# Performance work log

Hardware: AMD Instinct MI355X
Metric: run time of the kernel (lower is better)

The kernel has to match this reference:

```python
import jax, jax.numpy as jnp
import numpy as np

D_MODEL = 1024
HEADS = 16
HEAD_DIM = D_MODEL // HEADS


def setup_inputs() -> dict:
    key = jax.random.key(0)
    ks = jax.random.split(key, 6)
    B, S, D = 2, 2048, D_MODEL
    scale = 1.0 / np.sqrt(D)
    x = jax.random.normal(ks[0], (B, S, D), dtype=jnp.float32)
    mask = jax.random.randint(ks[1], (B, S), 0, 2, dtype=jnp.int32)
    Wq = jax.random.normal(ks[2], (D, D), dtype=jnp.float32) * scale
    Wk = jax.random.normal(ks[3], (D, D), dtype=jnp.float32) * scale
    Wv = jax.random.normal(ks[4], (D, D), dtype=jnp.float32) * scale
    Wp = jax.random.normal(ks[5], (D, D), dtype=jnp.float32) * scale
    zb = jnp.zeros((D,), dtype=jnp.float32)
    return {"x": x, "mask": mask, "Wq": Wq, "bq": zb, "Wk": Wk, "bk": zb,
            "Wv": Wv, "bv": zb, "Wp": Wp, "bp": zb}


def reference(x, mask, Wq, bq, Wk, bk, Wv, bv, Wp, bp):
    B, S, D = x.shape
    H, Dh = HEADS, HEAD_DIM

    def split_heads(t):  # [B,S,D] -> [B,H,S,Dh]
        return t.reshape(B, S, H, Dh).transpose(0, 2, 1, 3)

    q = split_heads(x @ Wq + bq)
    k = split_heads(x @ Wk + bk)
    v = split_heads(x @ Wv + bv)

    att = jnp.einsum('bhqd,bhkd->bhqk', q, k) / jnp.sqrt(jnp.float32(Dh))
    # key-padding mask: [B,S] -> [B,1,1,S]; masked positions -> -inf
    m = (mask[:, None, None, :] != 0)
    att = jnp.where(m, att, -jnp.inf)
    att = jax.nn.softmax(att, axis=-1)
    # rows that were fully masked produce NaN -> zero them (masked_fill(isnan, 0))
    att = jnp.where(jnp.isnan(att), 0.0, att)

    y = jnp.einsum('bhqk,bhkd->bhqd', att, v)  # [B,H,S,Dh]
    y = y.transpose(0, 2, 1, 3).reshape(B, S, D)
    return y @ Wp + bp
```

## Files before the change

kernel.cpp:

```cpp
#include <hip/hip_runtime.h>
#include <math.h>

#define D_MODEL 1024
#define HEADS 16
#define HEAD_DIM 64
#define SEQ 2048
#define BATCH 2
#define KVT 64
#define QTILE 64
#define SCALE_Q 0.18033688f

typedef __attribute__((ext_vector_type(8))) short bf16x8;
typedef __attribute__((ext_vector_type(4))) float f32x4;

__device__ __forceinline__ short f2bf(float f) {
    union { float f; unsigned u; } v; v.f = f;
    unsigned r = (v.u + 0x7FFFu + ((v.u >> 16) & 1u)) >> 16;
    return (short)r;
}

__device__ __forceinline__ unsigned cvt_pk_bf16(float lo, float hi) {
    unsigned r;
    asm("v_cvt_pk_bf16_f32 %0, %1, %2" : "=v"(r) : "v"(lo), "v"(hi));
    return r;
}

__device__ __forceinline__ float fexp2(float x) {
    float r;
    asm("v_exp_f32 %0, %1" : "=v"(r) : "v"(x));
    return r;
}

__global__ __launch_bounds__(256) void prep(
    const float* __restrict__ x, const float* __restrict__ Wq,
    const float* __restrict__ Wk, const float* __restrict__ Wv,
    const float* __restrict__ Wp, const int* __restrict__ mask,
    short* __restrict__ xb, short* __restrict__ Wqkvt,
    short* __restrict__ Wpt, float* __restrict__ maskf) {
    __shared__ float t[32][33];
    const int bid = blockIdx.x;
    if (bid < 2048) {
        const int i = bid * 256 + threadIdx.x;
        float4 a = ((const float4*)x)[2 * i];
        float4 b = ((const float4*)x)[2 * i + 1];
        short r[8] = {f2bf(a.x), f2bf(a.y), f2bf(a.z), f2bf(a.w),
                      f2bf(b.x), f2bf(b.y), f2bf(b.z), f2bf(b.w)};
        *(uint4*)(xb + 8 * i) = *(uint4*)r;
    } else if (bid < 6144) {
        const int tt = bid - 2048;
        const int z = tt >> 10;
        const int rem = tt & 1023;
        const float* W = z == 0 ? Wq : z == 1 ? Wk : z == 2 ? Wv : Wp;
        short* dst = (z < 3) ? Wqkvt + (size_t)z * 1024 * 1024 : Wpt;
        const int n0 = (rem & 31) * 32, k0 = (rem >> 5) * 32;
        const int tx = threadIdx.x & 31, ty = threadIdx.x >> 5;
#pragma unroll
        for (int j = 0; j < 4; ++j)
            t[ty + j * 8][tx] = W[(size_t)(k0 + ty + j * 8) * 1024 + n0 + tx];
        __syncthreads();
#pragma unroll
        for (int j = 0; j < 4; ++j) {
            const int n = ty + j * 8;
            dst[(size_t)(n0 + n) * 1024 + k0 + tx] = f2bf(t[tx][n]);
        }
    } else {
        const int i = (bid - 6144) * 256 + threadIdx.x;
        maskf[i] = mask[i] ? 0.f : -INFINITY;
    }
}

template <int MODE>
__global__ __launch_bounds__(256) void mfma_gemm(
    const short* __restrict__ A, const short* __restrict__ Bt,
    const float* __restrict__ b0, const float* __restrict__ b1,
    const float* __restrict__ b2, float* __restrict__ outf,
    short* __restrict__ o0, short* __restrict__ o1, short* __restrict__ o2,
    int M, int N, int K) {
    __shared__ short As[2 * 128 * 32];
    __shared__ short Bs[2 * 128 * 32];

    const int tid = threadIdx.x;
    const int wave = tid >> 6, lane = tid & 63;
    const int l15 = lane & 15, lhi = lane >> 4;
    const int wm = wave >> 1, wn = wave & 1;

    const int nwgx = gridDim.x;
    const int nwg = nwgx * gridDim.y;
    const int lin = blockIdx.y * nwgx + blockIdx.x;
    const int swz = (lin & 7) * (nwg >> 3) + (lin >> 3);
    const int bm0 = (swz / nwgx) * 128, bn0 = (swz % nwgx) * 128;

    f32x4 acc[4][4];
#pragma unroll
    for (int m = 0; m < 4; ++m)
#pragma unroll
        for (int n = 0; n < 4; ++n) acc[m][n] = (f32x4){0.f, 0.f, 0.f, 0.f};

#define STAGE_G(buf, kt_)                                                         \
    {                                                                             \
        const int k0 = (kt_) * 32;                                                \
        _Pragma("unroll") for (int p = 0; p < 2; ++p) {                           \
            const int o = (wave * 2 + p) * 64 + lane;                             \
            const int r = o >> 2;                                                 \
            const int gs = (o & 3) ^ ((r >> 1) & 3);                              \
            __builtin_amdgcn_global_load_lds(                                     \
                (const __attribute__((address_space(1))) void*)(                  \
                    A + (size_t)(bm0 + r) * K + k0 + gs * 8),                     \
                (__attribute__((address_space(3))) void*)(                        \
                    As + (size_t)(buf) * 4096 + (wave * 2 + p) * 512),            \
                16, 0, 0);                                                        \
            __builtin_amdgcn_global_load_lds(                                     \
                (const __attribute__((address_space(1))) void*)(                  \
                    Bt + (size_t)(bn0 + r) * K + k0 + gs * 8),                    \
                (__attribute__((address_space(3))) void*)(                        \
                    Bs + (size_t)(buf) * 4096 + (wave * 2 + p) * 512),            \
                16, 0, 0);                                                        \
        }                                                                         \
    }

    const int NT = K / 32;
    STAGE_G(0, 0);
    __syncthreads();
    for (int kt = 0; kt < NT; ++kt) {
        const int cur = kt & 1;
        if (kt + 1 < NT) STAGE_G((kt + 1) & 1, kt + 1);
        bf16x8 af[4], bf[4];
        const int sg = (lhi ^ ((l15 >> 1) & 3)) * 16;
#pragma unroll
        for (int m = 0; m < 4; ++m)
            af[m] = *(const bf16x8*)((char*)As + cur * 8192 +
                                     (wm * 64 + m * 16 + l15) * 64 + sg);
#pragma unroll
        for (int n = 0; n < 4; ++n)
            bf[n] = *(const bf16x8*)((char*)Bs + cur * 8192 +
                                     (wn * 64 + n * 16 + l15) * 64 + sg);
        __builtin_amdgcn_s_setprio(1);
#pragma unroll
        for (int m = 0; m < 4; ++m)
#pragma unroll
            for (int n = 0; n < 4; ++n)
                acc[m][n] = __builtin_amdgcn_mfma_f32_16x16x32_bf16(af[m], bf[n], acc[m][n], 0, 0, 0);
        __builtin_amdgcn_s_setprio(0);
        __syncthreads();
    }
#undef STAGE_G

    const int which = (MODE == 1) ? (bn0 >> 10) : 0;
#pragma unroll
    for (int m = 0; m < 4; ++m) {
#pragma unroll
        for (int n = 0; n < 4; ++n) {
            const int col = bn0 + wn * 64 + n * 16 + l15;
            if (MODE == 0) {
#pragma unroll
                for (int rr = 0; rr < 4; ++rr) {
                    const int row = bm0 + wm * 64 + m * 16 + lhi * 4 + rr;
                    outf[(size_t)row * N + col] = acc[m][n][rr] + b0[col];
                }
            } else {
                const int cc = col & 1023;
                const int h = cc >> 6, dh = cc & 63;
                const int row0 = bm0 + wm * 64 + m * 16 + lhi * 4;
                const int b = row0 >> 11, s0 = row0 & (SEQ - 1);
                if (which == 2) {
                    const float bias = b2[cc];
                    uint2 w;
                    w.x = cvt_pk_bf16(acc[m][n][0] + bias, acc[m][n][1] + bias);
                    w.y = cvt_pk_bf16(acc[m][n][2] + bias, acc[m][n][3] + bias);
                    *(uint2*)(o2 + ((size_t)(b * HEADS + h) * HEAD_DIM + dh) * SEQ + s0) = w;
                } else {
                    const float bias = (which == 0 ? b0 : b1)[cc];
                    short* dst = which == 0 ? o0 : o1;
#pragma unroll
                    for (int rr = 0; rr < 4; ++rr) {
                        float v = acc[m][n][rr] + bias;
                        if (which == 0) v *= SCALE_Q;
                        dst[(((size_t)(b * HEADS + h)) * SEQ + s0 + rr) * HEAD_DIM + dh] = f2bf(v);
                    }
                }
            }
        }
    }
}

__global__ __launch_bounds__(256, 4) void flash_attn(
    const short* __restrict__ Q, const short* __restrict__ K,
    const short* __restrict__ Vt, const float* __restrict__ maskf,
    short* __restrict__ Y) {
    __shared__ unsigned char kt[2][KVT * 128];
    __shared__ unsigned char vt[2][HEAD_DIM * 128];
    __shared__ unsigned char pb[4][16 * 128];

    const int tid = threadIdx.x;
    const int wave = tid >> 6;
    const int lane = tid & 63;
    const int l15 = lane & 15;
    const int lhi = lane >> 4;

    const int nwg = gridDim.x;
    const int wg = blockIdx.x;
    const int swz = (wg & 7) * (nwg >> 3) + (wg >> 3);
    const int qt = swz & 31;
    const int bh = swz >> 5;
    const int b = bh >> 4;

    const int q0 = qt * QTILE + wave * 16;

    const short* Qp = Q + ((size_t)bh * SEQ + q0 + l15) * HEAD_DIM;
    bf16x8 qf[2];
    qf[0] = *(const bf16x8*)(Qp + 8 * lhi);
    qf[1] = *(const bf16x8*)(Qp + 8 * lhi + 32);

    const unsigned char* Kb8 = (const unsigned char*)(K + (size_t)bh * SEQ * HEAD_DIM);
    const unsigned char* Vb8 = (const unsigned char*)(Vt + (size_t)bh * HEAD_DIM * SEQ);
    const float* mb = maskf + b * SEQ;

#define STAGE(buf, kvi)                                                            \
    {                                                                              \
        const unsigned char* kbase = Kb8 + (size_t)(kvi) * KVT * 128;              \
        const unsigned char* vbase = Vb8 + (size_t)(kvi) * 128;                    \
        _Pragma("unroll") for (int p = 0; p < 2; ++p) {                            \
            const int o = (wave * 2 + p) * 64 + lane;                              \
            const int row = o >> 3;                                                \
            const int inner = (o & 7) * 16;                                        \
            const int src = inner ^ ((row & 7) << 4);                              \
            __builtin_amdgcn_global_load_lds(                                      \
                (const __attribute__((address_space(1))) void*)(                   \
                    kbase + row * 128 + src),                                      \
                (__attribute__((address_space(3))) void*)(                         \
                    &kt[buf][(wave * 2 + p) * 1024]),                              \
                16, 0, 0);                                                         \
            __builtin_amdgcn_global_load_lds(                                      \
                (const __attribute__((address_space(1))) void*)(                   \
                    vbase + (size_t)row * (SEQ * 2) + src),                        \
                (__attribute__((address_space(3))) void*)(                         \
                    &vt[buf][(wave * 2 + p) * 1024]),                              \
                16, 0, 0);                                                         \
        }                                                                          \
    }

    f32x4 accO[4];
    float mrow = -30000.f, lrow = 0.f;
#pragma unroll
    for (int i = 0; i < 4; ++i) accO[i] = (f32x4){0.f, 0.f, 0.f, 0.f};

    STAGE(0, 0);
    __syncthreads();

    for (int kv = 0; kv < SEQ / KVT; ++kv) {
        const int cur = kv & 1;
        if (kv + 1 < SEQ / KVT) STAGE((kv + 1) & 1, kv + 1);

        const int k0 = kv * KVT;

        f32x4 accS[4];
#pragma unroll
        for (int nt = 0; nt < 4; ++nt) accS[nt] = (f32x4){0.f, 0.f, 0.f, 0.f};
#pragma unroll
        for (int c = 0; c < 2; ++c) {
            bf16x8 kf[4];
#pragma unroll
            for (int nt = 0; nt < 4; ++nt) {
                const int key = l15 + 16 * nt;
                kf[nt] = *(const bf16x8*)(kt[cur] + key * 128 +
                                          ((16 * lhi + 64 * c) ^ ((key & 7) << 4)));
            }
            __builtin_amdgcn_s_setprio(1);
#pragma unroll
            for (int nt = 0; nt < 4; ++nt)
                accS[nt] = __builtin_amdgcn_mfma_f32_16x16x32_bf16(kf[nt], qf[c], accS[nt], 0, 0, 0);
            __builtin_amdgcn_s_setprio(0);
        }

#pragma unroll
        for (int nt = 0; nt < 4; ++nt) {
            const f32x4 ma = *(const f32x4*)(mb + k0 + 16 * nt + 4 * lhi);
#pragma unroll
            for (int r = 0; r < 4; ++r) accS[nt][r] += ma[r];
        }

        float t0 = fmaxf(fmaxf(accS[0][0], accS[0][1]), fmaxf(accS[0][2], accS[0][3]));
        float t1 = fmaxf(fmaxf(accS[1][0], accS[1][1]), fmaxf(accS[1][2], accS[1][3]));
        float t2 = fmaxf(fmaxf(accS[2][0], accS[2][1]), fmaxf(accS[2][2], accS[2][3]));
        float t3 = fmaxf(fmaxf(accS[3][0], accS[3][1]), fmaxf(accS[3][2], accS[3][3]));
        float smax = fmaxf(fmaxf(t0, t1), fmaxf(t2, t3));
        smax = fmaxf(smax, __shfl_xor(smax, 16));
        smax = fmaxf(smax, __shfl_xor(smax, 32));

        if (!__all(smax <= mrow + 11.5f)) {
            const float mn = fmaxf(mrow, smax);
            const float alpha = fexp2(mrow - mn);
            lrow *= alpha;
#pragma unroll
            for (int d = 0; d < 4; ++d)
#pragma unroll
                for (int r = 0; r < 4; ++r) accO[d][r] *= alpha;
            mrow = mn;
        }

        float rs = 0.f;
#pragma unroll
        for (int nt = 0; nt < 4; ++nt)
#pragma unroll
            for (int r = 0; r < 4; ++r) {
                const float pv = fexp2(accS[nt][r] - mrow);
                accS[nt][r] = pv;
                rs += pv;
            }
        rs += __shfl_xor(rs, 16);
        rs += __shfl_xor(rs, 32);
        lrow += rs;

#pragma unroll
        for (int nt = 0; nt < 4; ++nt) {
            uint2 w;
            w.x = cvt_pk_bf16(accS[nt][0], accS[nt][1]);
            w.y = cvt_pk_bf16(accS[nt][2], accS[nt][3]);
            *(uint2*)(pb[wave] + l15 * 128 + ((32 * nt + 8 * lhi) ^ (l15 << 3))) = w;
        }

#pragma unroll
        for (int c = 0; c < 2; ++c) {
            union { bf16x8 v; uint2 u[2]; } pfu;
            pfu.u[0] = *(const uint2*)(pb[wave] + l15 * 128 +
                                       ((16 * lhi + 64 * c) ^ (l15 << 3)));
            pfu.u[1] = *(const uint2*)(pb[wave] + l15 * 128 +
                                       ((16 * lhi + 64 * c + 8) ^ (l15 << 3)));
            const bf16x8 pf = pfu.v;
            bf16x8 vf[4];
#pragma unroll
            for (int d = 0; d < 4; ++d) {
                const int dh = l15 + 16 * d;
                vf[d] = *(const bf16x8*)(vt[cur] + dh * 128 +
                                         ((16 * lhi + 64 * c) ^ ((dh & 7) << 4)));
            }
            __builtin_amdgcn_s_setprio(1);
#pragma unroll
            for (int d = 0; d < 4; ++d)
                accO[d] = __builtin_amdgcn_mfma_f32_16x16x32_bf16(vf[d], pf, accO[d], 0, 0, 0);
            __builtin_amdgcn_s_setprio(0);
        }
        __syncthreads();
    }
#undef STAGE

    const float inv = (lrow > 0.f) ? 1.f / lrow : 0.f;
    const int qg = q0 + l15;
    short* Yp = Y + ((size_t)b * SEQ + qg) * D_MODEL + (bh & 15) * HEAD_DIM;
#pragma unroll
    for (int d = 0; d < 4; ++d) {
        uint2 w;
        w.x = cvt_pk_bf16(accO[d][0] * inv, accO[d][1] * inv);
        w.y = cvt_pk_bf16(accO[d][2] * inv, accO[d][3] * inv);
        *(uint2*)(Yp + 16 * d + 4 * lhi) = w;
    }
}

extern "C" void kernel_launch(void* const* d_in, const int* in_sizes, int n_in,
                              void* d_out, int out_size, void* d_ws, size_t ws_size,
                              hipStream_t stream) {
    const float* x    = (const float*)d_in[0];
    const int*   mask = (const int*)  d_in[1];
    const float* Wq   = (const float*)d_in[2];
    const float* bq   = (const float*)d_in[3];
    const float* Wk   = (const float*)d_in[4];
    const float* bk   = (const float*)d_in[5];
    const float* Wv   = (const float*)d_in[6];
    const float* bv   = (const float*)d_in[7];
    const float* Wp   = (const float*)d_in[8];
    const float* bp   = (const float*)d_in[9];
    float* out = (float*)d_out;

    short* ws    = (short*)d_ws;
    short* xb    = ws;
    short* Wqkvt = xb + ((size_t)4 << 20);
    short* Wpt   = Wqkvt + ((size_t)3 << 20);
    short* Qb    = Wpt + ((size_t)1 << 20);
    short* Kb    = Qb + ((size_t)4 << 20);
    short* Vtb   = Kb + ((size_t)4 << 20);
    short* Yb    = Vtb + ((size_t)4 << 20);
    float* maskf = (float*)(Yb + ((size_t)4 << 20));

    const int M = BATCH * SEQ;

    prep<<<dim3(6160), 256, 0, stream>>>(x, Wq, Wk, Wv, Wp, mask,
                                         xb, Wqkvt, Wpt, maskf);

    mfma_gemm<1><<<dim3(3 * D_MODEL / 128, M / 128), 256, 0, stream>>>(
        xb, Wqkvt, bq, bk, bv, nullptr, Qb, Kb, Vtb, M, 3 * D_MODEL, D_MODEL);

    flash_attn<<<dim3(BATCH * HEADS * (SEQ / QTILE)), 256, 0, stream>>>(Qb, Kb, Vtb, maskf, Yb);

    mfma_gemm<0><<<dim3(D_MODEL / 128, M / 128), 256, 0, stream>>>(
        Yb, Wpt, bp, bp, bp, out, nullptr, nullptr, nullptr, M, D_MODEL, D_MODEL);
}
```

Measured before the change: 134.5 us.

## Process two 16-row query subtiles per wave in flash attention

Doubles the query tile per workgroup to 128, so each wave handles 32 query rows as two 16-row subtiles. The K and V fragments read from LDS are reused across both subtiles, halving LDS reads and the staging traffic per unit of MFMA work. The cost is more registers (two sets of accumulators and softmax state), a lower occupancy target in the launch bounds, a larger P buffer, and half as many workgroups. The grid size must match the new QTILE.

```diff
diff --git a/kernel.cpp b/kernel.cpp
--- a/kernel.cpp
+++ b/kernel.cpp
@@ -7,7 +7,7 @@
 #define SEQ 2048
 #define BATCH 2
 #define KVT 64
-#define QTILE 64
+#define QTILE 128
 #define SCALE_Q 0.18033688f
 
 typedef __attribute__((ext_vector_type(8))) short bf16x8;
@@ -183,13 +183,13 @@
     }
 }
 
-__global__ __launch_bounds__(256, 4) void flash_attn(
+__global__ __launch_bounds__(256, 2) void flash_attn(
     const short* __restrict__ Q, const short* __restrict__ K,
     const short* __restrict__ Vt, const float* __restrict__ maskf,
     short* __restrict__ Y) {
     __shared__ unsigned char kt[2][KVT * 128];
     __shared__ unsigned char vt[2][HEAD_DIM * 128];
-    __shared__ unsigned char pb[4][16 * 128];
+    __shared__ unsigned char pb[4][32 * 128];
 
     const int tid = threadIdx.x;
     const int wave = tid >> 6;
@@ -200,16 +200,19 @@
     const int nwg = gridDim.x;
     const int wg = blockIdx.x;
     const int swz = (wg & 7) * (nwg >> 3) + (wg >> 3);
-    const int qt = swz & 31;
-    const int bh = swz >> 5;
+    const int qt = swz & 15;
+    const int bh = swz >> 4;
     const int b = bh >> 4;
 
-    const int q0 = qt * QTILE + wave * 16;
-
-    const short* Qp = Q + ((size_t)bh * SEQ + q0 + l15) * HEAD_DIM;
-    bf16x8 qf[2];
-    qf[0] = *(const bf16x8*)(Qp + 8 * lhi);
-    qf[1] = *(const bf16x8*)(Qp + 8 * lhi + 32);
+    const int q0 = qt * QTILE + wave * 32;
+
+    bf16x8 qf[2][2];
+#pragma unroll
+    for (int qi = 0; qi < 2; ++qi) {
+        const short* Qp = Q + ((size_t)bh * SEQ + q0 + 16 * qi + l15) * HEAD_DIM;
+        qf[qi][0] = *(const bf16x8*)(Qp + 8 * lhi);
+        qf[qi][1] = *(const bf16x8*)(Qp + 8 * lhi + 32);
+    }
 
     const unsigned char* Kb8 = (const unsigned char*)(K + (size_t)bh * SEQ * HEAD_DIM);
     const unsigned char* Vb8 = (const unsigned char*)(Vt + (size_t)bh * HEAD_DIM * SEQ);
@@ -239,10 +242,12 @@
         }                                                                          \
     }
 
-    f32x4 accO[4];
-    float mrow = -30000.f, lrow = 0.f;
-#pragma unroll
-    for (int i = 0; i < 4; ++i) accO[i] = (f32x4){0.f, 0.f, 0.f, 0.f};
+    f32x4 accO[2][4];
+    float mrow[2] = {-30000.f, -30000.f}, lrow[2] = {0.f, 0.f};
+#pragma unroll
+    for (int qi = 0; qi < 2; ++qi)
+#pragma unroll
+        for (int i = 0; i < 4; ++i) accO[qi][i] = (f32x4){0.f, 0.f, 0.f, 0.f};
 
     STAGE(0, 0);
     __syncthreads();
@@ -253,9 +258,11 @@
 
         const int k0 = kv * KVT;
 
-        f32x4 accS[4];
-#pragma unroll
-        for (int nt = 0; nt < 4; ++nt) accS[nt] = (f32x4){0.f, 0.f, 0.f, 0.f};
+        f32x4 accS[2][4];
+#pragma unroll
+        for (int qi = 0; qi < 2; ++qi)
+#pragma unroll
+            for (int nt = 0; nt < 4; ++nt) accS[qi][nt] = (f32x4){0.f, 0.f, 0.f, 0.f};
 #pragma unroll
         for (int c = 0; c < 2; ++c) {
             bf16x8 kf[4];
@@ -267,66 +274,81 @@
             }
             __builtin_amdgcn_s_setprio(1);
 #pragma unroll
+            for (int qi = 0; qi < 2; ++qi)
+#pragma unroll
+                for (int nt = 0; nt < 4; ++nt)
+                    accS[qi][nt] = __builtin_amdgcn_mfma_f32_16x16x32_bf16(
+                        kf[nt], qf[qi][c], accS[qi][nt], 0, 0, 0);
+            __builtin_amdgcn_s_setprio(0);
+        }
+
+        f32x4 ma[4];
+#pragma unroll
+        for (int nt = 0; nt < 4; ++nt)
+            ma[nt] = *(const f32x4*)(mb + k0 + 16 * nt + 4 * lhi);
+#pragma unroll
+        for (int qi = 0; qi < 2; ++qi)
+#pragma unroll
             for (int nt = 0; nt < 4; ++nt)
-                accS[nt] = __builtin_amdgcn_mfma_f32_16x16x32_bf16(kf[nt], qf[c], accS[nt], 0, 0, 0);
-            __builtin_amdgcn_s_setprio(0);
-        }
-
-#pragma unroll
-        for (int nt = 0; nt < 4; ++nt) {
-            const f32x4 ma = *(const f32x4*)(mb + k0 + 16 * nt + 4 * lhi);
-#pragma unroll
-            for (int r = 0; r < 4; ++r) accS[nt][r] += ma[r];
-        }
-
-        float t0 = fmaxf(fmaxf(accS[0][0], accS[0][1]), fmaxf(accS[0][2], accS[0][3]));
-        float t1 = fmaxf(fmaxf(accS[1][0], accS[1][1]), fmaxf(accS[1][2], accS[1][3]));
-        float t2 = fmaxf(fmaxf(accS[2][0], accS[2][1]), fmaxf(accS[2][2], accS[2][3]));
-        float t3 = fmaxf(fmaxf(accS[3][0], accS[3][1]), fmaxf(accS[3][2], accS[3][3]));
-        float smax = fmaxf(fmaxf(t0, t1), fmaxf(t2, t3));
-        smax = fmaxf(smax, __shfl_xor(smax, 16));
-        smax = fmaxf(smax, __shfl_xor(smax, 32));
-
-        if (!__all(smax <= mrow + 11.5f)) {
-            const float mn = fmaxf(mrow, smax);
-            const float alpha = fexp2(mrow - mn);
-            lrow *= alpha;
-#pragma unroll
-            for (int d = 0; d < 4; ++d)
-#pragma unroll
-                for (int r = 0; r < 4; ++r) accO[d][r] *= alpha;
-            mrow = mn;
-        }
-
-        float rs = 0.f;
-#pragma unroll
-        for (int nt = 0; nt < 4; ++nt)
-#pragma unroll
-            for (int r = 0; r < 4; ++r) {
-                const float pv = fexp2(accS[nt][r] - mrow);
-                accS[nt][r] = pv;
-                rs += pv;
-            }
-        rs += __shfl_xor(rs, 16);
-        rs += __shfl_xor(rs, 32);
-        lrow += rs;
-
-#pragma unroll
-        for (int nt = 0; nt < 4; ++nt) {
-            uint2 w;
-            w.x = cvt_pk_bf16(accS[nt][0], accS[nt][1]);
-            w.y = cvt_pk_bf16(accS[nt][2], accS[nt][3]);
-            *(uint2*)(pb[wave] + l15 * 128 + ((32 * nt + 8 * lhi) ^ (l15 << 3))) = w;
+#pragma unroll
+                for (int r = 0; r < 4; ++r) accS[qi][nt][r] += ma[nt][r];
+
+#pragma unroll
+        for (int qi = 0; qi < 2; ++qi) {
+            float t0 = fmaxf(fmaxf(accS[qi][0][0], accS[qi][0][1]), fmaxf(accS[qi][0][2], accS[qi][0][3]));
+            float t1 = fmaxf(fmaxf(accS[qi][1][0], accS[qi][1][1]), fmaxf(accS[qi][1][2], accS[qi][1][3]));
+            float t2 = fmaxf(fmaxf(accS[qi][2][0], accS[qi][2][1]), fmaxf(accS[qi][2][2], accS[qi][2][3]));
+            float t3 = fmaxf(fmaxf(accS[qi][3][0], accS[qi][3][1]), fmaxf(accS[qi][3][2], accS[qi][3][3]));
+            float smax = fmaxf(fmaxf(t0, t1), fmaxf(t2, t3));
+            smax = fmaxf(smax, __shfl_xor(smax, 16));
+            smax = fmaxf(smax, __shfl_xor(smax, 32));
+
+            if (!__all(smax <= mrow[qi] + 11.5f)) {
+                const float mn = fmaxf(mrow[qi], smax);
+                const float alpha = fexp2(mrow[qi] - mn);
+                lrow[qi] *= alpha;
+#pragma unroll
+                for (int d = 0; d < 4; ++d)
+#pragma unroll
+                    for (int r = 0; r < 4; ++r) accO[qi][d][r] *= alpha;
+                mrow[qi] = mn;
+            }
+
+            float rs = 0.f;
+#pragma unroll
+            for (int nt = 0; nt < 4; ++nt)
+#pragma unroll
+                for (int r = 0; r < 4; ++r) {
+                    const float pv = fexp2(accS[qi][nt][r] - mrow[qi]);
+                    accS[qi][nt][r] = pv;
+                    rs += pv;
+                }
+            rs += __shfl_xor(rs, 16);
+            rs += __shfl_xor(rs, 32);
+            lrow[qi] += rs;
+
+#pragma unroll
+            for (int nt = 0; nt < 4; ++nt) {
+                uint2 w;
+                w.x = cvt_pk_bf16(accS[qi][nt][0], accS[qi][nt][1]);
+                w.y = cvt_pk_bf16(accS[qi][nt][2], accS[qi][nt][3]);
+                *(uint2*)(pb[wave] + (l15 + 16 * qi) * 128 +
+                          ((32 * nt + 8 * lhi) ^ (l15 << 3))) = w;
+            }
         }
 
 #pragma unroll
         for (int c = 0; c < 2; ++c) {
-            union { bf16x8 v; uint2 u[2]; } pfu;
-            pfu.u[0] = *(const uint2*)(pb[wave] + l15 * 128 +
-                                       ((16 * lhi + 64 * c) ^ (l15 << 3)));
-            pfu.u[1] = *(const uint2*)(pb[wave] + l15 * 128 +
-                                       ((16 * lhi + 64 * c + 8) ^ (l15 << 3)));
-            const bf16x8 pf = pfu.v;
+            bf16x8 pf[2];
+#pragma unroll
+            for (int qi = 0; qi < 2; ++qi) {
+                union { bf16x8 v; uint2 u[2]; } pfu;
+                pfu.u[0] = *(const uint2*)(pb[wave] + (l15 + 16 * qi) * 128 +
+                                           ((16 * lhi + 64 * c) ^ (l15 << 3)));
+                pfu.u[1] = *(const uint2*)(pb[wave] + (l15 + 16 * qi) * 128 +
+                                           ((16 * lhi + 64 * c + 8) ^ (l15 << 3)));
+                pf[qi] = pfu.v;
+            }
             bf16x8 vf[4];
 #pragma unroll
             for (int d = 0; d < 4; ++d) {
@@ -336,23 +358,29 @@
             }
             __builtin_amdgcn_s_setprio(1);
 #pragma unroll
-            for (int d = 0; d < 4; ++d)
-                accO[d] = __builtin_amdgcn_mfma_f32_16x16x32_bf16(vf[d], pf, accO[d], 0, 0, 0);
+            for (int qi = 0; qi < 2; ++qi)
+#pragma unroll
+                for (int d = 0; d < 4; ++d)
+                    accO[qi][d] = __builtin_amdgcn_mfma_f32_16x16x32_bf16(
+                        vf[d], pf[qi], accO[qi][d], 0, 0, 0);
             __builtin_amdgcn_s_setprio(0);
         }
         __syncthreads();
     }
 #undef STAGE
 
-    const float inv = (lrow > 0.f) ? 1.f / lrow : 0.f;
-    const int qg = q0 + l15;
-    short* Yp = Y + ((size_t)b * SEQ + qg) * D_MODEL + (bh & 15) * HEAD_DIM;
-#pragma unroll
-    for (int d = 0; d < 4; ++d) {
-        uint2 w;
-        w.x = cvt_pk_bf16(accO[d][0] * inv, accO[d][1] * inv);
-        w.y = cvt_pk_bf16(accO[d][2] * inv, accO[d][3] * inv);
-        *(uint2*)(Yp + 16 * d + 4 * lhi) = w;
+#pragma unroll
+    for (int qi = 0; qi < 2; ++qi) {
+        const float inv = (lrow[qi] > 0.f) ? 1.f / lrow[qi] : 0.f;
+        const int qg = q0 + 16 * qi + l15;
+        short* Yp = Y + ((size_t)b * SEQ + qg) * D_MODEL + (bh & 15) * HEAD_DIM;
+#pragma unroll
+        for (int d = 0; d < 4; ++d) {
+            uint2 w;
+            w.x = cvt_pk_bf16(accO[qi][d][0] * inv, accO[qi][d][1] * inv);
+            w.y = cvt_pk_bf16(accO[qi][d][2] * inv, accO[qi][d][3] * inv);
+            *(uint2*)(Yp + 16 * d + 4 * lhi) = w;
+        }
     }
 }
 
```

Measured after the change: 134.6 us. No clear change (+0.1%).
